# Kernel optimization log

Measured on AMD Instinct MI355X. Metric: run time of the kernel, lower is better.

Reference implementation:

```python
import jax, jax.numpy as jnp
import numpy as np

COST_CLASS, COST_BBOX, COST_GIOU = 1.0, 5.0, 2.0
BS, Q, K, T = 16, 1024, 256, 128


def setup_inputs() -> dict:
    key = jax.random.key(0)
    k1, k2, k3, k4 = jax.random.split(key, 4)
    pred_logits = jax.random.normal(k1, (BS, Q, K), dtype=jnp.float32)
    # predicted boxes in (mid, width) format, width > 0
    pred_boxes = jax.random.uniform(k2, (BS, Q, 2), dtype=jnp.float32, minval=0.05, maxval=1.0)
    # target boxes in (x0, x1) format with x0 < x1
    tgt_boxes = jnp.sort(jax.random.uniform(k3, (BS, T, 2), dtype=jnp.float32), axis=-1)
    tgt_labels = jax.random.randint(k4, (BS, T), 0, K, dtype=jnp.int32)
    return {"pred_logits": pred_logits, "pred_boxes": pred_boxes,
            "tgt_boxes": tgt_boxes, "tgt_labels": tgt_labels}


def midwtoxy(x):
    mid, w = x[..., 0], x[..., 1]
    return jnp.stack([mid - 0.5 * w, mid + 0.5 * w], axis=-1)


def getgiou(b1, b2):
    # b1: [N,2] (x0,x1), b2: [M,2]; returns [N,M] generalized IoU for 1-D intervals
    area1 = b1[:, 1] - b1[:, 0]              # [N]
    area2 = b2[:, 1] - b2[:, 0]              # [M]
    lt = jnp.maximum(b1[:, None, 0], b2[None, :, 0])
    rb = jnp.minimum(b1[:, None, 1], b2[None, :, 1])
    inter = jnp.clip(rb - lt, 0.0)           # [N,M]
    union = area1[:, None] + area2[None, :] - inter
    iou = inter / union
    hull_lt = jnp.minimum(b1[:, None, 0], b2[None, :, 0])
    hull_rb = jnp.maximum(b1[:, None, 1], b2[None, :, 1])
    hull = jnp.clip(hull_rb - hull_lt, 0.0)
    return iou - (hull - union) / hull


def reference(pred_logits, pred_boxes, tgt_boxes, tgt_labels):
    bs, q, k = pred_logits.shape
    out_prob = jax.nn.softmax(pred_logits.reshape(bs * q, k), axis=-1)  # [bs*Q, K]
    out_bbox = midwtoxy(pred_boxes.reshape(bs * q, 2))                  # [bs*Q, 2] (x0,x1)
    tgt_bbox = tgt_boxes.reshape(-1, 2)                                 # [bs*T, 2]
    tgt_ids = tgt_labels.reshape(-1)                                    # [bs*T]

    cost_class = -out_prob[:, tgt_ids]                                  # [bs*Q, bs*T]
    # L1 cdist over 2 coords, without materializing a [N,M,2] tensor
    cost_bbox = (jnp.abs(out_bbox[:, None, 0] - tgt_bbox[None, :, 0]) +
                 jnp.abs(out_bbox[:, None, 1] - tgt_bbox[None, :, 1]))
    cost_giou = -getgiou(out_bbox, tgt_bbox)

    C = COST_BBOX * cost_bbox + COST_CLASS * cost_class + COST_GIOU * cost_giou
    # [bs, Q, bs*T]; the original feeds the per-sample diagonal blocks
    # C[b, :, b*T:(b+1)*T] to scipy linear_sum_assignment (CPU, non-differentiable,
    # excluded from this GPU-math baseline).
    return C.reshape(bs, q, -1)
```

## Files before the change

kernel.cpp:

```cpp
#include <hip/hip_runtime.h>

#define BS 16
#define Q  1024
#define K  256
#define T  128
#define NROWS (BS * Q)
#define M     (BS * T)
#define RPB   16

__device__ __forceinline__ float cost_fn(float x0, float x1, float w1,
                                         float tx0, float tx1, float w2,
                                         float p) {
    float l1   = fabsf(x0 - tx0) + fabsf(x1 - tx1);
    float ir   = fminf(x1, tx1) - fmaxf(x0, tx0);
    float s    = w1 + w2;
    float inter= fmaxf(ir, 0.0f);
    float mn   = fminf(ir, 0.0f);
    float uni  = s - inter;
    float hull = s - ir;
    float giou = (inter * hull + mn * uni) * __builtin_amdgcn_rcpf(uni * hull);
    return fmaf(5.0f, l1, -p) - 2.0f * giou;
}

__global__ __launch_bounds__(256, 4) void hungarian_cost_kernel(
    const float* __restrict__ pred_logits,
    const float* __restrict__ pred_boxes,
    const float* __restrict__ tgt_boxes,
    const int*   __restrict__ tgt_labels,
    float* __restrict__ out)
{
    __shared__ float probs[RPB][K];
    __shared__ float rbox[RPB][3];

    const int t    = threadIdx.x;
    const int w    = t >> 6;
    const int lane = t & 63;
    const int row0 = blockIdx.x * RPB;

    if (t < RPB) {
        float2 mw = ((const float2*)pred_boxes)[row0 + t];
        rbox[t][0] = mw.x - 0.5f * mw.y;
        rbox[t][1] = mw.x + 0.5f * mw.y;
        rbox[t][2] = mw.y;
    }

    #pragma unroll
    for (int r = 0; r < 4; ++r) {
        int lr = 4 * w + r;
        int n  = row0 + lr;
        float4 v = ((const float4*)(pred_logits + (size_t)n * K))[lane];
        float e0 = __expf(v.x), e1 = __expf(v.y), e2 = __expf(v.z), e3 = __expf(v.w);
        float sum = (e0 + e1) + (e2 + e3);
        #pragma unroll
        for (int off = 1; off < 64; off <<= 1)
            sum += __shfl_xor(sum, off, 64);
        float rs = __builtin_amdgcn_rcpf(sum);
        float4 pv; pv.x = e0 * rs; pv.y = e1 * rs; pv.z = e2 * rs; pv.w = e3 * rs;
        ((float4*)&probs[lr][0])[lane] = pv;
    }
    __syncthreads();

    const float4* tb4 = (const float4*)tgt_boxes;
    const int4*   tl4 = (const int4*)tgt_labels;

    float4 B01[2], B23[2];
    int4   LAB[2];
    float  W2[2][4];
    #pragma unroll
    for (int g = 0; g < 2; ++g) {
        int vv = t + g * 256;
        B01[g] = tb4[2 * vv];
        B23[g] = tb4[2 * vv + 1];
        LAB[g] = tl4[vv];
        W2[g][0] = B01[g].y - B01[g].x;
        W2[g][1] = B01[g].w - B01[g].z;
        W2[g][2] = B23[g].y - B23[g].x;
        W2[g][3] = B23[g].w - B23[g].z;
    }

    #pragma unroll
    for (int chunk = 0; chunk < 2; ++chunk) {
        float rx0[8], rx1[8], rw1[8];
        #pragma unroll
        for (int r = 0; r < 8; ++r) {
            int lr = chunk * 8 + r;
            rx0[r] = rbox[lr][0]; rx1[r] = rbox[lr][1]; rw1[r] = rbox[lr][2];
        }
        #pragma unroll
        for (int g = 0; g < 2; ++g) {
            int vv = t + g * 256;
            #pragma unroll
            for (int r = 0; r < 8; ++r) {
                int lr = chunk * 8 + r;
                const float* prow = &probs[lr][0];
                float4 rr;
                rr.x = cost_fn(rx0[r], rx1[r], rw1[r], B01[g].x, B01[g].y, W2[g][0], prow[LAB[g].x]);
                rr.y = cost_fn(rx0[r], rx1[r], rw1[r], B01[g].z, B01[g].w, W2[g][1], prow[LAB[g].y]);
                rr.z = cost_fn(rx0[r], rx1[r], rw1[r], B23[g].x, B23[g].y, W2[g][2], prow[LAB[g].z]);
                rr.w = cost_fn(rx0[r], rx1[r], rw1[r], B23[g].z, B23[g].w, W2[g][3], prow[LAB[g].w]);
                ((float4*)(out + (size_t)(row0 + lr) * M))[vv] = rr;
            }
        }
    }
}

extern "C" void kernel_launch(void* const* d_in, const int* in_sizes, int n_in,
                              void* d_out, int out_size, void* d_ws, size_t ws_size,
                              hipStream_t stream) {
    const float* pred_logits = (const float*)d_in[0];
    const float* pred_boxes  = (const float*)d_in[1];
    const float* tgt_boxes   = (const float*)d_in[2];
    const int*   tgt_labels  = (const int*)d_in[3];
    float* out = (float*)d_out;

    hungarian_cost_kernel<<<NROWS / RPB, 256, 0, stream>>>(
        pred_logits, pred_boxes, tgt_boxes, tgt_labels, out);
}
```

Baseline: 150.2 us.

## Transpose probability tile in LDS and use nontemporal loads/stores

```diff
diff --git a/kernel.cpp b/kernel.cpp
--- a/kernel.cpp
+++ b/kernel.cpp
@@ -7,6 +7,9 @@
 #define NROWS (BS * Q)
 #define M     (BS * T)
 #define RPB   16
+#define PSTR  20
+
+typedef float f32x4 __attribute__((ext_vector_type(4)));
 
 __device__ __forceinline__ float cost_fn(float x0, float x1, float w1,
                                          float tx0, float tx1, float w2,
@@ -29,7 +32,7 @@
     const int*   __restrict__ tgt_labels,
     float* __restrict__ out)
 {
-    __shared__ float probs[RPB][K];
+    __shared__ __align__(16) float probsT[K][PSTR];
     __shared__ float rbox[RPB][3];
 
     const int t    = threadIdx.x;
@@ -44,19 +47,31 @@
         rbox[t][2] = mw.y;
     }
 
+    f32x4 pv[4];
     #pragma unroll
     for (int r = 0; r < 4; ++r) {
-        int lr = 4 * w + r;
-        int n  = row0 + lr;
-        float4 v = ((const float4*)(pred_logits + (size_t)n * K))[lane];
+        int n = row0 + 4 * w + r;
+        f32x4 v = __builtin_nontemporal_load(
+            ((const f32x4*)(pred_logits + (size_t)n * K)) + lane);
         float e0 = __expf(v.x), e1 = __expf(v.y), e2 = __expf(v.z), e3 = __expf(v.w);
         float sum = (e0 + e1) + (e2 + e3);
         #pragma unroll
         for (int off = 1; off < 64; off <<= 1)
             sum += __shfl_xor(sum, off, 64);
         float rs = __builtin_amdgcn_rcpf(sum);
-        float4 pv; pv.x = e0 * rs; pv.y = e1 * rs; pv.z = e2 * rs; pv.w = e3 * rs;
-        ((float4*)&probs[lr][0])[lane] = pv;
+        pv[r].x = e0 * rs; pv[r].y = e1 * rs; pv[r].z = e2 * rs; pv[r].w = e3 * rs;
+    }
+    {
+        const float* p0 = (const float*)&pv[0];
+        const float* p1 = (const float*)&pv[1];
+        const float* p2 = (const float*)&pv[2];
+        const float* p3 = (const float*)&pv[3];
+        #pragma unroll
+        for (int j = 0; j < 4; ++j) {
+            f32x4 cv;
+            cv.x = p0[j]; cv.y = p1[j]; cv.z = p2[j]; cv.w = p3[j];
+            *(f32x4*)&probsT[4 * lane + j][4 * w] = cv;
+        }
     }
     __syncthreads();
 
@@ -64,14 +79,18 @@
     const int4*   tl4 = (const int4*)tgt_labels;
 
     float4 B01[2], B23[2];
-    int4   LAB[2];
     float  W2[2][4];
+    const float* pl[2][4];
     #pragma unroll
     for (int g = 0; g < 2; ++g) {
         int vv = t + g * 256;
         B01[g] = tb4[2 * vv];
         B23[g] = tb4[2 * vv + 1];
-        LAB[g] = tl4[vv];
+        int4 L = tl4[vv];
+        pl[g][0] = &probsT[L.x][0];
+        pl[g][1] = &probsT[L.y][0];
+        pl[g][2] = &probsT[L.z][0];
+        pl[g][3] = &probsT[L.w][0];
         W2[g][0] = B01[g].y - B01[g].x;
         W2[g][1] = B01[g].w - B01[g].z;
         W2[g][2] = B23[g].y - B23[g].x;
@@ -79,26 +98,34 @@
     }
 
     #pragma unroll
-    for (int chunk = 0; chunk < 2; ++chunk) {
-        float rx0[8], rx1[8], rw1[8];
+    for (int ch = 0; ch < 4; ++ch) {
+        float rx0[4], rx1[4], rw1[4];
         #pragma unroll
-        for (int r = 0; r < 8; ++r) {
-            int lr = chunk * 8 + r;
+        for (int r = 0; r < 4; ++r) {
+            int lr = 4 * ch + r;
             rx0[r] = rbox[lr][0]; rx1[r] = rbox[lr][1]; rw1[r] = rbox[lr][2];
         }
         #pragma unroll
         for (int g = 0; g < 2; ++g) {
             int vv = t + g * 256;
+            float4 P0 = *(const float4*)(pl[g][0] + 4 * ch);
+            float4 P1 = *(const float4*)(pl[g][1] + 4 * ch);
+            float4 P2 = *(const float4*)(pl[g][2] + 4 * ch);
+            float4 P3 = *(const float4*)(pl[g][3] + 4 * ch);
+            const float* q0 = (const float*)&P0;
+            const float* q1 = (const float*)&P1;
+            const float* q2 = (const float*)&P2;
+            const float* q3 = (const float*)&P3;
             #pragma unroll
-            for (int r = 0; r < 8; ++r) {
-                int lr = chunk * 8 + r;
-                const float* prow = &probs[lr][0];
-                float4 rr;
-                rr.x = cost_fn(rx0[r], rx1[r], rw1[r], B01[g].x, B01[g].y, W2[g][0], prow[LAB[g].x]);
-                rr.y = cost_fn(rx0[r], rx1[r], rw1[r], B01[g].z, B01[g].w, W2[g][1], prow[LAB[g].y]);
-                rr.z = cost_fn(rx0[r], rx1[r], rw1[r], B23[g].x, B23[g].y, W2[g][2], prow[LAB[g].z]);
-                rr.w = cost_fn(rx0[r], rx1[r], rw1[r], B23[g].z, B23[g].w, W2[g][3], prow[LAB[g].w]);
-                ((float4*)(out + (size_t)(row0 + lr) * M))[vv] = rr;
+            for (int r = 0; r < 4; ++r) {
+                int lr = 4 * ch + r;
+                f32x4 rr;
+                rr.x = cost_fn(rx0[r], rx1[r], rw1[r], B01[g].x, B01[g].y, W2[g][0], q0[r]);
+                rr.y = cost_fn(rx0[r], rx1[r], rw1[r], B01[g].z, B01[g].w, W2[g][1], q1[r]);
+                rr.z = cost_fn(rx0[r], rx1[r], rw1[r], B23[g].x, B23[g].y, W2[g][2], q2[r]);
+                rr.w = cost_fn(rx0[r], rx1[r], rw1[r], B23[g].z, B23[g].w, W2[g][3], q3[r]);
+                __builtin_nontemporal_store(
+                    rr, ((f32x4*)(out + (size_t)(row0 + lr) * M)) + vv);
             }
         }
     }
```

New measurement: 163.2 us. 1.09x slower.
